# Optimization experiments

Hardware: AMD Instinct MI355X
Metric: run time of the kernel (lower is better)

Reference implementation:

```python
import jax, jax.numpy as jnp
import numpy as np

N = 50000          # nodes
E = 800000         # edges (COO)
IN_CH = 128
H1, H2, OUT = 200, 100, 2   # 100*out, 50*out, out with out_channels=2
EPS = 1e-12
DROP_P = 0.1


def setup_inputs() -> dict:
    key = jax.random.key(0)
    ks = jax.random.split(key, 6)
    x = jax.random.normal(ks[0], (N, IN_CH), dtype=jnp.float32)
    edge_index = jax.random.randint(ks[1], (2, E), 0, N)
    W1 = jax.random.normal(ks[2], (IN_CH, H1), dtype=jnp.float32) / np.sqrt(IN_CH)
    W2 = jax.random.normal(ks[3], (H1, H2), dtype=jnp.float32) / np.sqrt(H1)
    W3 = jax.random.normal(ks[4], (H2, OUT), dtype=jnp.float32) / np.sqrt(H2)
    beta1 = jnp.float32(1.0)
    beta2 = jnp.float32(1.0)
    beta3 = jnp.float32(1.0)
    return dict(x=x, edge_index=edge_index, W1=W1, W2=W2, W3=W3,
                beta1=beta1, beta2=beta2, beta3=beta3)


def _agnn_layer(x, W, beta, src, dst):
    # project in -> out channels, then AGNN cosine-attention propagation
    h = x @ W                                               # [N, D]
    hn = h / jnp.maximum(jnp.linalg.norm(h, axis=-1, keepdims=True), EPS)
    a = beta * jnp.sum(hn[src] * hn[dst], axis=-1)          # [E'] edge logits
    amax = jax.ops.segment_max(a, dst, num_segments=N)      # stable segment softmax
    amax = jnp.where(jnp.isfinite(amax), amax, 0.0)
    e = jnp.exp(a - amax[dst])
    denom = jax.ops.segment_sum(e, dst, num_segments=N)
    alpha = e / jnp.maximum(denom[dst], EPS)
    return jax.ops.segment_sum(h[src] * alpha[:, None], dst, num_segments=N)


def _dropout(k, x, p=DROP_P):
    keep = jax.random.bernoulli(k, 1.0 - p, x.shape)
    return jnp.where(keep, x / (1.0 - p), 0.0)


def reference(x, edge_index, W1, W2, W3, beta1, beta2, beta3):
    src, dst = edge_index[0], edge_index[1]
    loop = jnp.arange(N)                                    # self-loops (AGNNConv default)
    src = jnp.concatenate([src, loop])
    dst = jnp.concatenate([dst, loop])
    k1, k2 = jax.random.split(jax.random.key(42))
    h = jax.nn.relu(_agnn_layer(x, W1, beta1, src, dst))
    h = _dropout(k1, h)
    h = jax.nn.relu(_agnn_layer(h, W2, beta2, src, dst))
    h = _dropout(k2, h)
    h = jax.nn.relu(_agnn_layer(h, W3, beta3, src, dst))
    return h
```

## Files before the change

### kernel.cpp

```cpp
#include <hip/hip_runtime.h>
#include <hip/hip_bf16.h>

#define NN 50000
#define NE 800000
#define EPSN 1e-12f


#define H_OFF    0ull
#define A_OFF    40000000ull
#define H3_OFF   80000000ull
#define RINV_OFF 80400000ull
#define OFFS_OFF 80600000ull
#define DEG_OFF  80800016ull
#define CURS_OFF 81000016ull
#define ESRC_OFF 81200016ull
#define CHNK_OFF 84600016ull

__host__ __device__ inline void tf20(unsigned k0, unsigned k1, unsigned& x0, unsigned& x1) {
  unsigned ks2 = k0 ^ k1 ^ 0x1BD11BDAu;
  x0 += k0; x1 += k1;
#define TFR(r) { x0 += x1; x1 = ((x1 << (r)) | (x1 >> (32 - (r)))) ^ x0; }
  TFR(13) TFR(15) TFR(26) TFR(6)
  x0 += k1;  x1 += ks2 + 1u;
  TFR(17) TFR(29) TFR(16) TFR(24)
  x0 += ks2; x1 += k0 + 2u;
  TFR(13) TFR(15) TFR(26) TFR(6)
  x0 += k0;  x1 += k1 + 3u;
  TFR(17) TFR(29) TFR(16) TFR(24)
  x0 += k1;  x1 += ks2 + 4u;
  TFR(13) TFR(15) TFR(26) TFR(6)
  x0 += ks2; x1 += k0 + 5u;
#undef TFR
}

__device__ __forceinline__ float dropf(float val, unsigned k0, unsigned k1, unsigned i) {
  unsigned x0 = 0u, x1 = i;
  tf20(k0, k1, x0, x1);
  unsigned bits = x0 ^ x1;
  float u = __uint_as_float((bits >> 9) | 0x3F800000u) - 1.0f;
  return (u < 0.9f) ? val * (1.0f / 0.9f) : 0.0f;
}

__device__ __forceinline__ float wave_sum(float x) {
  x += __shfl_xor(x, 32); x += __shfl_xor(x, 16); x += __shfl_xor(x, 8);
  x += __shfl_xor(x, 4);  x += __shfl_xor(x, 2);  x += __shfl_xor(x, 1);
  return x;
}

template<int K, int KT, int NLP, int N>
__device__ __forceinline__ void gemm_core4(float* __restrict__ As, float* __restrict__ Ws,
                                           const float* __restrict__ A,
                                           const float* __restrict__ W,
                                           float* __restrict__ H,
                                           float* __restrict__ RINV, int M, int row0) {
  static_assert(NLP % 64 == 0 && KT % 4 == 0, "layout");
  constexpr int KTP = KT + 1, NV = N / 4, NC = NLP / 64, PD4 = NLP / 4 - NV;
  const float4* A4 = (const float4*)A;
  const float4* W4 = (const float4*)W;
  const float4* Ws4 = (const float4*)Ws;

  int t = threadIdx.x, rgrp = t >> 4, cg = t & 15;
  float acc[4][NC * 4];
#pragma unroll
  for (int rr = 0; rr < 4; rr++)
#pragma unroll
    for (int j = 0; j < NC * 4; j++) acc[rr][j] = 0.f;

  for (int k0 = 0; k0 < K; k0 += KT) {
    __syncthreads();
    for (int idx = t; idx < 64 * (KT / 4); idx += 256) {
      int r = idx / (KT / 4), cq = idx - r * (KT / 4);
      int gr = row0 + r;
      float4 v = (gr < M) ? A4[(size_t)gr * (K / 4) + (k0 / 4) + cq]
                          : make_float4(0.f, 0.f, 0.f, 0.f);
      float* dst = &As[r * KTP + cq * 4];
      dst[0] = v.x; dst[1] = v.y; dst[2] = v.z; dst[3] = v.w;
    }
    for (int idx = t; idx < KT * NV; idx += 256) {
      int kk = idx / NV, cq = idx - kk * NV;
      *(float4*)&Ws[kk * NLP + cq * 4] = W4[(size_t)(k0 + kk) * NV + cq];
    }
    for (int idx = t; idx < KT * PD4; idx += 256) {
      int kk = idx / PD4, pq = idx - kk * PD4;
      *(float4*)&Ws[kk * NLP + N + pq * 4] = make_float4(0.f, 0.f, 0.f, 0.f);
    }
    __syncthreads();
#pragma unroll
    for (int kk = 0; kk < KT; kk++) {
      float a[4];
#pragma unroll
      for (int rr = 0; rr < 4; rr++) a[rr] = As[(rgrp * 4 + rr) * KTP + kk];
#pragma unroll
      for (int q = 0; q < NC; q++) {
        float4 wv = Ws4[kk * (NLP / 4) + cg + 16 * q];
#pragma unroll
        for (int rr = 0; rr < 4; rr++) {
          acc[rr][q * 4 + 0] = fmaf(a[rr], wv.x, acc[rr][q * 4 + 0]);
          acc[rr][q * 4 + 1] = fmaf(a[rr], wv.y, acc[rr][q * 4 + 1]);
          acc[rr][q * 4 + 2] = fmaf(a[rr], wv.z, acc[rr][q * 4 + 2]);
          acc[rr][q * 4 + 3] = fmaf(a[rr], wv.w, acc[rr][q * 4 + 3]);
        }
      }
    }
  }

  int r0 = row0 + rgrp * 4;
#pragma unroll
  for (int rr = 0; rr < 4; rr++) {
    int gr = r0 + rr;
    float ss = 0.f;
#pragma unroll
    for (int q = 0; q < NC; q++) {
#pragma unroll
      for (int j = 0; j < 4; j++) {
        float v = acc[rr][q * 4 + j];
        ss += v * v;
        int c = 4 * (cg + 16 * q) + j;
        if (gr < M && c < N) H[(size_t)gr * N + c] = v;
      }
    }
    ss += __shfl_xor(ss, 1); ss += __shfl_xor(ss, 2);
    ss += __shfl_xor(ss, 4); ss += __shfl_xor(ss, 8);
    if (cg == 0 && gr < M) RINV[gr] = 1.0f / fmaxf(sqrtf(ss), EPSN);
  }
}

__global__ __launch_bounds__(256, 4) void gemm1a_hist_kernel(
    const float* __restrict__ X, const float* __restrict__ W1,
    float* __restrict__ H, float* __restrict__ RINV,
    const int* __restrict__ EI, int* __restrict__ DEG) {
  __shared__ float As[64 * 17];
  __shared__ float Ws[16 * 256];
  int bid = blockIdx.x;
  if (bid < 391) {
    gemm_core4<128, 16, 256, 200>(As, Ws, X, W1, H, RINV, NN, bid * 64);
  } else {
    for (int e = (bid - 391) * 256 + threadIdx.x; e < NE; e += 242 * 256)
      atomicAdd(&DEG[EI[NE + e]], 1);
  }
}

__global__ __launch_bounds__(256, 4) void gemm1b_scat_kernel(
    const float* __restrict__ X, const float* __restrict__ W1,
    float* __restrict__ H, float* __restrict__ RINV,
    const int* __restrict__ EI, int* __restrict__ CURS,
    int* __restrict__ ESRC) {
  __shared__ float As[64 * 17];
  __shared__ float Ws[16 * 256];
  int bid = blockIdx.x;
  if (bid < 391) {
    gemm_core4<128, 16, 256, 200>(As, Ws, X, W1, H, RINV, NN, (bid + 391) * 64);
  } else {
    for (int e = (bid - 391) * 256 + threadIdx.x; e < NE; e += 242 * 256) {
      int s = EI[e], d = EI[NE + e];
      int pos = atomicAdd(&CURS[d], 1);
      ESRC[pos] = s;
    }
  }
}

__global__ __launch_bounds__(256, 4) void gemm2_kernel(const float* __restrict__ A,
                                                       const float* __restrict__ W,
                                                       float* __restrict__ H,
                                                       float* __restrict__ RINV, int M) {
  __shared__ float As[64 * 41];
  __shared__ float Ws[40 * 128];
  gemm_core4<200, 40, 128, 100>(As, Ws, A, W, H, RINV, M, blockIdx.x * 64);
}

__global__ __launch_bounds__(256) void csr_scan1_kernel(const int* __restrict__ deg,
                                                        int* __restrict__ offs,
                                                        int* __restrict__ chunk) {
  __shared__ int lds[8];
  int t = threadIdx.x;
  int base = blockIdx.x * 1024 + t * 4;
  int d[4];
#pragma unroll
  for (int j = 0; j < 4; j++) d[j] = (base + j < NN) ? deg[base + j] : 0;
  int ts = d[0] + d[1] + d[2] + d[3];
  int lane = t & 63, wave = t >> 6;
  int inc = ts;
#pragma unroll
  for (int sh = 1; sh < 64; sh <<= 1) { int u = __shfl_up(inc, sh); if (lane >= sh) inc += u; }
  if (lane == 63) lds[wave] = inc;
  __syncthreads();
  if (t == 0) { int s = 0; for (int w = 0; w < 4; w++) { int x = lds[w]; lds[w] = s; s += x; } lds[4] = s; }
  __syncthreads();
  int p = lds[wave] + inc - ts;
#pragma unroll
  for (int j = 0; j < 4; j++) { if (base + j < NN) offs[base + j] = p; p += d[j]; }
  if (t == 255) chunk[blockIdx.x] = lds[4];
}

__global__ __launch_bounds__(64) void csr_scan2_kernel(int* __restrict__ chunk) {
  int t = threadIdx.x;
  int v = (t < 49) ? chunk[t] : 0;
  int inc = v;
#pragma unroll
  for (int sh = 1; sh < 64; sh <<= 1) { int u = __shfl_up(inc, sh); if (t >= sh) inc += u; }
  if (t < 49) chunk[t] = inc - v;
}

__global__ __launch_bounds__(256) void csr_scan3_kernel(int* __restrict__ offs,
                                                        const int* __restrict__ chunk,
                                                        int* __restrict__ curs) {
  int i = blockIdx.x * 256 + threadIdx.x;
  if (i < NN) {
    int val = offs[i] + chunk[i >> 10];
    offs[i] = val;
    curs[i] = val;
  }
  if (i == 0) offs[NN] = NE;
}

template<int D, int VEC, bool DROP>
__device__ __forceinline__ void attn_body(const float* __restrict__ H,
                                          const float* __restrict__ RINV,
                                          const int* __restrict__ OFFS,
                                          const int* __restrict__ ESRC,
                                          const float* __restrict__ BETA,
                                          float* __restrict__ OUT,
                                          unsigned k0, unsigned k1) {
  constexpr int NL = D / VEC;
  int v = blockIdx.x * 4 + (threadIdx.x >> 6);
  int lane = threadIdx.x & 63;
  bool act = lane < NL;
  float beta = BETA[0];
  float bd = beta * RINV[v];
  int e0 = OFFS[v], e1 = OFFS[v + 1];

  float wself = __expf(beta);
  float s = wself;
  float hd[VEC], acc[VEC];
  if (act) {
    const float* hrow = H + (size_t)v * D + lane * VEC;
    if (VEC == 4) { float4 tv = *(const float4*)hrow; hd[0] = tv.x; hd[1] = tv.y; hd[2] = tv.z; hd[3] = tv.w; }
    else          { float2 tv = *(const float2*)hrow; hd[0] = tv.x; hd[1] = tv.y; }
#pragma unroll
    for (int j = 0; j < VEC; j++) acc[j] = wself * hd[j];
  }

  int idx = e0;
  for (; idx + 4 <= e1; idx += 4) {
    int   u[4];
    float r[4], dt[4], hs[4][VEC];
#pragma unroll
    for (int m = 0; m < 4; m++) u[m] = ESRC[idx + m];
#pragma unroll
    for (int m = 0; m < 4; m++) r[m] = RINV[u[m]];
    float dd[4] = {0.f, 0.f, 0.f, 0.f};
    if (act) {
#pragma unroll
      for (int m = 0; m < 4; m++) {
        const float* p = H + (size_t)u[m] * D + lane * VEC;
        if (VEC == 4) { float4 a = *(const float4*)p; hs[m][0] = a.x; hs[m][1] = a.y; hs[m][2] = a.z; hs[m][3] = a.w; }
        else          { float2 a = *(const float2*)p; hs[m][0] = a.x; hs[m][1] = a.y; }
      }
#pragma unroll
      for (int m = 0; m < 4; m++)
#pragma unroll
        for (int j = 0; j < VEC; j++) dd[m] = fmaf(hd[j], hs[m][j], dd[m]);
    }
#pragma unroll
    for (int m = 0; m < 4; m++) dt[m] = wave_sum(dd[m]);
    float w[4];
#pragma unroll
    for (int m = 0; m < 4; m++) { w[m] = __expf(bd * dt[m] * r[m]); s += w[m]; }
    if (act) {
#pragma unroll
      for (int m = 0; m < 4; m++)
#pragma unroll
        for (int j = 0; j < VEC; j++) acc[j] = fmaf(w[m], hs[m][j], acc[j]);
    }
  }
  for (; idx < e1; ++idx) {
    int u0 = ESRC[idx];
    float r0 = RINV[u0];
    float h0[VEC];
    float ddt = 0.f;
    if (act) {
      const float* p0 = H + (size_t)u0 * D + lane * VEC;
      if (VEC == 4) { float4 a = *(const float4*)p0; h0[0] = a.x; h0[1] = a.y; h0[2] = a.z; h0[3] = a.w; }
      else          { float2 a = *(const float2*)p0; h0[0] = a.x; h0[1] = a.y; }
#pragma unroll
      for (int j = 0; j < VEC; j++) ddt = fmaf(hd[j], h0[j], ddt);
    }
    ddt = wave_sum(ddt);
    float w0 = __expf(bd * ddt * r0);
    s += w0;
    if (act) {
#pragma unroll
      for (int j = 0; j < VEC; j++) acc[j] = fmaf(w0, h0[j], acc[j]);
    }
  }

  float rs = 1.0f / fmaxf(s, EPSN);
  if (act) {
    float o[VEC];
#pragma unroll
    for (int j = 0; j < VEC; j++) {
      float val = acc[j] * rs;
      val = (val <= 0.0f) ? 0.0f : val;
      if (DROP) val = dropf(val, k0, k1, (unsigned)(v * D + lane * VEC + j));
      o[j] = val;
    }
    float* orow = OUT + (size_t)v * D + lane * VEC;
    if (VEC == 4) *(float4*)orow = make_float4(o[0], o[1], o[2], o[3]);
    else          *(float2*)orow = make_float2(o[0], o[1]);
  }
}

__global__ __launch_bounds__(256) void attn1_kernel(const float* H, const float* RINV,
                                                    const int* OFFS, const int* ESRC,
                                                    const float* BETA, float* OUT,
                                                    unsigned k0, unsigned k1) {
  attn_body<200, 4, true>(H, RINV, OFFS, ESRC, BETA, OUT, k0, k1);
}

__global__ __launch_bounds__(256) void attn2_proj_kernel(
    const float* __restrict__ H, const float* __restrict__ RINV,
    const int* __restrict__ OFFS, const int* __restrict__ ESRC,
    const float* __restrict__ BETA, const float* __restrict__ W3,
    float* __restrict__ H3, float* __restrict__ RINV3,
    unsigned k0, unsigned k1) {
  constexpr int D = 100, VEC = 2, NL = 50;
  int v = blockIdx.x * 4 + (threadIdx.x >> 6);
  int lane = threadIdx.x & 63;
  bool act = lane < NL;
  float beta = BETA[0];
  float bd = beta * RINV[v];
  int e0 = OFFS[v], e1 = OFFS[v + 1];

  float4 w3v = make_float4(0.f, 0.f, 0.f, 0.f);
  if (act) w3v = *(const float4*)&W3[4 * lane];

  float wself = __expf(beta);
  float s = wself;
  float hd[VEC], acc[VEC];
  if (act) {
    const float* hrow = H + (size_t)v * D + lane * VEC;
    float2 tv = *(const float2*)hrow; hd[0] = tv.x; hd[1] = tv.y;
#pragma unroll
    for (int j = 0; j < VEC; j++) acc[j] = wself * hd[j];
  }

  int idx = e0;
  for (; idx + 4 <= e1; idx += 4) {
    int   u[4];
    float r[4], dt[4], hs[4][VEC];
#pragma unroll
    for (int m = 0; m < 4; m++) u[m] = ESRC[idx + m];
#pragma unroll
    for (int m = 0; m < 4; m++) r[m] = RINV[u[m]];
    float dd[4] = {0.f, 0.f, 0.f, 0.f};
    if (act) {
#pragma unroll
      for (int m = 0; m < 4; m++) {
        const float* p = H + (size_t)u[m] * D + lane * VEC;
        float2 a = *(const float2*)p; hs[m][0] = a.x; hs[m][1] = a.y;
      }
#pragma unroll
      for (int m = 0; m < 4; m++)
#pragma unroll
        for (int j = 0; j < VEC; j++) dd[m] = fmaf(hd[j], hs[m][j], dd[m]);
    }
#pragma unroll
    for (int m = 0; m < 4; m++) dt[m] = wave_sum(dd[m]);
    float w[4];
#pragma unroll
    for (int m = 0; m < 4; m++) { w[m] = __expf(bd * dt[m] * r[m]); s += w[m]; }
    if (act) {
#pragma unroll
      for (int m = 0; m < 4; m++)
#pragma unroll
        for (int j = 0; j < VEC; j++) acc[j] = fmaf(w[m], hs[m][j], acc[j]);
    }
  }
  for (; idx < e1; ++idx) {
    int u0 = ESRC[idx];
    float r0 = RINV[u0];
    float h0[VEC];
    float ddt = 0.f;
    if (act) {
      const float* p0 = H + (size_t)u0 * D + lane * VEC;
      float2 a = *(const float2*)p0; h0[0] = a.x; h0[1] = a.y;
#pragma unroll
      for (int j = 0; j < VEC; j++) ddt = fmaf(hd[j], h0[j], ddt);
    }
    ddt = wave_sum(ddt);
    float w0 = __expf(bd * ddt * r0);
    s += w0;
    if (act) {
#pragma unroll
      for (int j = 0; j < VEC; j++) acc[j] = fmaf(w0, h0[j], acc[j]);
    }
  }

  float rs = 1.0f / fmaxf(s, EPSN);
  float p0 = 0.f, p1 = 0.f;
  if (act) {
    float o[VEC];
#pragma unroll
    for (int j = 0; j < VEC; j++) {
      float val = acc[j] * rs;
      val = (val <= 0.0f) ? 0.0f : val;
      val = dropf(val, k0, k1, (unsigned)(v * D + lane * VEC + j));
      o[j] = val;
    }
    p0 = o[0] * w3v.x + o[1] * w3v.z;
    p1 = o[0] * w3v.y + o[1] * w3v.w;
  }
  p0 = wave_sum(p0);
  p1 = wave_sum(p1);
  if (lane == 0) {
    H3[2 * v] = p0; H3[2 * v + 1] = p1;
    RINV3[v] = 1.0f / fmaxf(sqrtf(p0 * p0 + p1 * p1), EPSN);
  }
}

__global__ __launch_bounds__(256) void attn3_kernel(const float* __restrict__ H3,
                                                    const float* __restrict__ RINV3,
                                                    const int* __restrict__ OFFS,
                                                    const int* __restrict__ ESRC,
                                                    const float* __restrict__ BETA,
                                                    float* __restrict__ out) {
  int v = blockIdx.x * 4 + (threadIdx.x >> 6);
  int lane = threadIdx.x & 63;
  float beta = BETA[0];
  float bd = beta * RINV3[v];
  float h0 = H3[2 * v], h1 = H3[2 * v + 1];
  int e0 = OFFS[v], e1 = OFFS[v + 1];
  float s = 0.f, a0 = 0.f, a1 = 0.f;
  for (int idx = e0 + lane; idx < e1; idx += 64) {
    int u = ESRC[idx];
    float s0 = H3[2 * u], s1 = H3[2 * u + 1];
    float w = __expf(bd * (h0 * s0 + h1 * s1) * RINV3[u]);
    s += w; a0 = fmaf(w, s0, a0); a1 = fmaf(w, s1, a1);
  }
  s = wave_sum(s); a0 = wave_sum(a0); a1 = wave_sum(a1);
  if (lane == 0) {
    float wself = __expf(beta);
    s += wself; a0 = fmaf(wself, h0, a0); a1 = fmaf(wself, h1, a1);
    float rs = 1.0f / fmaxf(s, EPSN);
    float o0 = a0 * rs, o1 = a1 * rs;
    out[2 * v]     = (o0 <= 0.0f) ? 0.0f : o0;
    out[2 * v + 1] = (o1 <= 0.0f) ? 0.0f : o1;
  }
}

extern "C" void kernel_launch(void* const* d_in, const int* in_sizes, int n_in,
                              void* d_out, int out_size, void* d_ws, size_t ws_size,
                              hipStream_t stream) {
  const float* X  = (const float*)d_in[0];
  const int*   EI = (const int*)d_in[1];
  const float* W1 = (const float*)d_in[2];
  const float* W2 = (const float*)d_in[3];
  const float* W3 = (const float*)d_in[4];
  const float* B1 = (const float*)d_in[5];
  const float* B2 = (const float*)d_in[6];
  const float* B3 = (const float*)d_in[7];

  char* ws = (char*)d_ws;
  float* H     = (float*)(ws + H_OFF);
  float* A     = (float*)(ws + A_OFF);
  float* H3    = (float*)(ws + H3_OFF);
  float* RINV  = (float*)(ws + RINV_OFF);
  int* OFFS    = (int*)(ws + OFFS_OFF);
  int* DEG     = (int*)(ws + DEG_OFF);
  int* CURS    = (int*)(ws + CURS_OFF);
  float* RINV3 = (float*)(ws + CURS_OFF);
  int* ESRC    = (int*)(ws + ESRC_OFF);
  int* CHNK    = (int*)(ws + CHNK_OFF);

  unsigned k1a = 0u, k1b = 0u; tf20(0u, 42u, k1a, k1b);
  unsigned k2a = 0u, k2b = 1u; tf20(0u, 42u, k2a, k2b);

  hipMemsetAsync(DEG, 0, NN * sizeof(int), stream);

  gemm1a_hist_kernel<<<633, 256, 0, stream>>>(X, W1, H, RINV, EI, DEG);
  csr_scan1_kernel<<<49, 256, 0, stream>>>(DEG, OFFS, CHNK);
  csr_scan2_kernel<<<1, 64, 0, stream>>>(CHNK);
  csr_scan3_kernel<<<196, 256, 0, stream>>>(OFFS, CHNK, CURS);
  gemm1b_scat_kernel<<<633, 256, 0, stream>>>(X, W1, H, RINV, EI, CURS, ESRC);

  const int gb = (NN + 63) / 64;
  const int ab = NN / 4;

  attn1_kernel<<<ab, 256, 0, stream>>>(H, RINV, OFFS, ESRC, B1, A, k1a, k1b);
  gemm2_kernel<<<gb, 256, 0, stream>>>(A, W2, H, RINV, NN);
  attn2_proj_kernel<<<ab, 256, 0, stream>>>(H, RINV, OFFS, ESRC, B2, W3, H3, RINV3, k2a, k2b);
  attn3_kernel<<<ab, 256, 0, stream>>>(H3, RINV3, OFFS, ESRC, B3, (float*)d_out);
}
```

Before: 488.3 us.

## Run full GEMM1 alongside degree histogram, use standalone CSR scatter kernel

The first-layer GEMM now runs entirely in the kernel that also builds the degree histogram, with 782 GEMM blocks and 242 histogram blocks. Previously half of it was co-scheduled with the edge scatter. The scatter becomes a separate lightweight kernel with one thread per edge. This changes how GEMM work overlaps with the atomic-heavy CSR construction: the scatter no longer hides behind GEMM blocks, but gets a wider grid.

```diff
diff --git a/kernel.cpp b/kernel.cpp
--- a/kernel.cpp
+++ b/kernel.cpp
@@ -125,37 +125,18 @@
   }
 }
 
-__global__ __launch_bounds__(256, 4) void gemm1a_hist_kernel(
+__global__ __launch_bounds__(256, 4) void gemm1_hist_kernel(
     const float* __restrict__ X, const float* __restrict__ W1,
     float* __restrict__ H, float* __restrict__ RINV,
     const int* __restrict__ EI, int* __restrict__ DEG) {
   __shared__ float As[64 * 17];
   __shared__ float Ws[16 * 256];
   int bid = blockIdx.x;
-  if (bid < 391) {
+  if (bid < 782) {
     gemm_core4<128, 16, 256, 200>(As, Ws, X, W1, H, RINV, NN, bid * 64);
   } else {
-    for (int e = (bid - 391) * 256 + threadIdx.x; e < NE; e += 242 * 256)
+    for (int e = (bid - 782) * 256 + threadIdx.x; e < NE; e += 242 * 256)
       atomicAdd(&DEG[EI[NE + e]], 1);
-  }
-}
-
-__global__ __launch_bounds__(256, 4) void gemm1b_scat_kernel(
-    const float* __restrict__ X, const float* __restrict__ W1,
-    float* __restrict__ H, float* __restrict__ RINV,
-    const int* __restrict__ EI, int* __restrict__ CURS,
-    int* __restrict__ ESRC) {
-  __shared__ float As[64 * 17];
-  __shared__ float Ws[16 * 256];
-  int bid = blockIdx.x;
-  if (bid < 391) {
-    gemm_core4<128, 16, 256, 200>(As, Ws, X, W1, H, RINV, NN, (bid + 391) * 64);
-  } else {
-    for (int e = (bid - 391) * 256 + threadIdx.x; e < NE; e += 242 * 256) {
-      int s = EI[e], d = EI[NE + e];
-      int pos = atomicAdd(&CURS[d], 1);
-      ESRC[pos] = s;
-    }
   }
 }
 
@@ -211,6 +192,16 @@
     curs[i] = val;
   }
   if (i == 0) offs[NN] = NE;
+}
+
+__global__ __launch_bounds__(256) void csr_scatter_kernel(const int* __restrict__ ei,
+                                                          int* __restrict__ curs,
+                                                          int* __restrict__ esrc) {
+  int e = blockIdx.x * 256 + threadIdx.x;
+  if (e >= NE) return;
+  int s = ei[e], d = ei[NE + e];
+  int pos = atomicAdd(&curs[d], 1);
+  esrc[pos] = s;
 }
 
 template<int D, int VEC, bool DROP>
@@ -477,11 +468,11 @@
 
   hipMemsetAsync(DEG, 0, NN * sizeof(int), stream);
 
-  gemm1a_hist_kernel<<<633, 256, 0, stream>>>(X, W1, H, RINV, EI, DEG);
+  gemm1_hist_kernel<<<1024, 256, 0, stream>>>(X, W1, H, RINV, EI, DEG);
   csr_scan1_kernel<<<49, 256, 0, stream>>>(DEG, OFFS, CHNK);
   csr_scan2_kernel<<<1, 64, 0, stream>>>(CHNK);
   csr_scan3_kernel<<<196, 256, 0, stream>>>(OFFS, CHNK, CURS);
-  gemm1b_scat_kernel<<<633, 256, 0, stream>>>(X, W1, H, RINV, EI, CURS, ESRC);
+  csr_scatter_kernel<<<(NE + 255) / 256, 256, 0, stream>>>(EI, CURS, ESRC);
 
   const int gb = (NN + 63) / 64;
   const int ab = NN / 4;
```

Result: faster. 464.7 us (-4.8%).
